# Optimization experiments

Measured on AMD Instinct MI355X. Metric: run time of the kernel, lower is better.

The kernel has to match this reference:

```python
import jax, jax.numpy as jnp
import numpy as np

B, S, D = 4, 1024, 1024
H, DK, DV = 16, 64, 64


def setup_inputs() -> dict:
    key = jax.random.key(0)
    ks = jax.random.split(key, 8)
    sc = 0.02
    return {
        "queries": jax.random.normal(ks[0], (B, S, D), jnp.float32),
        "keys": jax.random.normal(ks[1], (B, S, D), jnp.float32),
        "values": jax.random.normal(ks[2], (B, S, D), jnp.float32),
        "attn_bias": jax.random.normal(ks[3], (B, 1, S, S), jnp.float32),
        "Wq": jax.random.normal(ks[4], (H * DK, D), jnp.float32) * sc,
        "Wk": jax.random.normal(ks[5], (H * DK, D), jnp.float32) * sc,
        "Wv": jax.random.normal(ks[6], (H * DV, D), jnp.float32) * sc,
        "Wp": jax.random.normal(ks[7], (D, H * DV), jnp.float32) * sc,
    }


def reference(queries, keys, values, attn_bias, Wq, Wk, Wv, Wp):
    # Linear (no bias): x @ W.T, then split heads -> [B, H, S, d]
    q = (queries @ Wq.T).reshape(B, S, H, DK).transpose(0, 2, 1, 3)
    k = (keys @ Wk.T).reshape(B, S, H, DK).transpose(0, 2, 1, 3)
    v = (values @ Wv.T).reshape(B, S, H, DV).transpose(0, 2, 1, 3)
    # NOTE: original scales by d_model**-0.5, not d_key**-0.5
    scores = jnp.einsum("bhqd,bhkd->bhqk", q, k) * (D ** -0.5)
    scores = scores + attn_bias  # bias broadcasts over heads
    weights = jax.nn.softmax(scores, axis=-1)
    out = jnp.einsum("bhqk,bhkd->bhqd", weights, v)  # [B,H,S,DV]
    out = out.transpose(0, 2, 1, 3).reshape(B, S, H * DV)
    return out @ Wp.T
```

## Files before the change

kernel.cpp:

```cpp
#include <hip/hip_runtime.h>
#include <hip/hip_bf16.h>

typedef unsigned short u16;
typedef unsigned int u32;
typedef __attribute__((ext_vector_type(8))) short bf16x8;
typedef __attribute__((ext_vector_type(8))) u16 u16x8;
typedef __attribute__((ext_vector_type(4))) u16 u16x4;
typedef __attribute__((ext_vector_type(4))) u32 u32x4;
typedef __attribute__((ext_vector_type(4))) float f32x4;
typedef __attribute__((ext_vector_type(16))) float f32x16;

typedef const __attribute__((address_space(1))) void* gas1_t;
typedef __attribute__((address_space(3))) void* las3_t;

#define MFMA16(a,b,c) __builtin_amdgcn_mfma_f32_16x16x32_bf16((a),(b),(c),0,0,0)
#define MFMA32(a,b,c) __builtin_amdgcn_mfma_f32_32x32x16_bf16((a),(b),(c),0,0,0)

static constexpr int BB = 4, SS = 1024, DD = 1024, HH = 16;

static __device__ __forceinline__ u16 f2b(float x) {
  union { __hip_bfloat16 h; u16 u; } cv;
  cv.h = __float2bfloat16(x);
  return cv.u;
}
static __device__ __forceinline__ u32 pk2(float a, float b) {
  return (u32)f2b(a) | ((u32)f2b(b) << 16);
}

__global__ __launch_bounds__(256) void cvt_all(
    const float* __restrict__ q, const float* __restrict__ k, const float* __restrict__ v,
    const float* __restrict__ wq_, const float* __restrict__ wk_, const float* __restrict__ wv_,
    const float* __restrict__ wp_,
    u16* __restrict__ qb, u16* __restrict__ kb, u16* __restrict__ vb,
    u16* __restrict__ wqb, u16* __restrict__ wkb, u16* __restrict__ wvb, u16* __restrict__ wpb) {
  int bid = blockIdx.x;
  const float* s; u16* d; int off;
  if      (bid < 4096)  { s = q;   d = qb;  off = bid; }
  else if (bid < 8192)  { s = k;   d = kb;  off = bid - 4096; }
  else if (bid < 12288) { s = v;   d = vb;  off = bid - 8192; }
  else if (bid < 13312) { s = wq_; d = wqb; off = bid - 12288; }
  else if (bid < 14336) { s = wk_; d = wkb; off = bid - 13312; }
  else if (bid < 15360) { s = wv_; d = wvb; off = bid - 14336; }
  else                  { s = wp_; d = wpb; off = bid - 15360; }
  int i = (off * 256 + threadIdx.x) * 4;
  float4 val = *(const float4*)(s + i);
  u16x4 r = { f2b(val.x), f2b(val.y), f2b(val.z), f2b(val.w) };
  *(u16x4*)(d + i) = r;
}

template<typename OT>
__global__ __launch_bounds__(256) void gemm_bt(
    const u16* __restrict__ Abase, const u16* __restrict__ Wbase, OT* __restrict__ Cbase,
    int N, int K, size_t sA, size_t sW, size_t sC) {
  const u16* A = Abase + (size_t)blockIdx.z * sA;
  const u16* W = Wbase + (size_t)blockIdx.z * sW;
  OT* C = Cbase + (size_t)blockIdx.z * sC;

  __shared__ __align__(16) u16 As[128 * 32];
  __shared__ __align__(16) u16 Bs[128 * 32];

  const int tid = threadIdx.x;
  const int lane = tid & 63;
  const int wid = tid >> 6;
  const int g = lane >> 4;
  const int li = lane & 15;
  const int brow = blockIdx.y * 128;
  const int bcol = blockIdx.x * 128;
  const int wr = (wid >> 1) * 64;
  const int wc = (wid & 1) * 64;

  const int srow = tid >> 2;
  const int scol = (tid & 3) * 8;

  f32x4 acc[4][4] = {};

  for (int k0 = 0; k0 < K; k0 += 32) {
#pragma unroll
    for (int c = 0; c < 2; ++c) {
      const u16* ga = A + (size_t)(brow + srow + c * 64) * K + k0 + scol;
      const u16* gw = W + (size_t)(bcol + srow + c * 64) * K + k0 + scol;
      __builtin_amdgcn_global_load_lds((gas1_t)(const void*)ga,
                                       (las3_t)(void*)(As + wid * 512 + c * 2048), 16, 0, 0);
      __builtin_amdgcn_global_load_lds((gas1_t)(const void*)gw,
                                       (las3_t)(void*)(Bs + wid * 512 + c * 2048), 16, 0, 0);
    }
    __syncthreads();

    bf16x8 a[4], b[4];
#pragma unroll
    for (int m = 0; m < 4; ++m)
      a[m] = *(const bf16x8*)&As[(wr + m * 16 + li) * 32 + g * 8];
#pragma unroll
    for (int n = 0; n < 4; ++n)
      b[n] = *(const bf16x8*)&Bs[(wc + n * 16 + li) * 32 + g * 8];
#pragma unroll
    for (int m = 0; m < 4; ++m)
#pragma unroll
      for (int n = 0; n < 4; ++n)
        acc[m][n] = MFMA16(a[m], b[n], acc[m][n]);
    __syncthreads();
  }

#pragma unroll
  for (int m = 0; m < 4; ++m)
#pragma unroll
    for (int n = 0; n < 4; ++n)
#pragma unroll
      for (int j = 0; j < 4; ++j) {
        int r = brow + wr + m * 16 + g * 4 + j;
        int c = bcol + wc + n * 16 + li;
        if constexpr (sizeof(OT) == 2) C[(size_t)r * N + c] = (OT)f2b(acc[m][n][j]);
        else                           C[(size_t)r * N + c] = acc[m][n][j];
      }
}

__global__ __launch_bounds__(256) void transpose_v(const u16* __restrict__ V, u16* __restrict__ Vt) {
  __shared__ __align__(16) u16 t[64][72];
  const int s0 = blockIdx.x * 64, h = blockIdx.y, b = blockIdx.z;
  const int tid = threadIdx.x;
#pragma unroll
  for (int it = 0; it < 2; ++it) {
    int slot = tid + it * 256;
    int r = slot >> 3, seg = slot & 7;
    *(u16x8*)&t[r][seg * 8] = *(const u16x8*)&V[(size_t)(b * SS + s0 + r) * DD + h * 64 + seg * 8];
  }
  __syncthreads();
#pragma unroll
  for (int it = 0; it < 2; ++it) {
    int slot = tid + it * 256;
    int dv = slot >> 3, seg = slot & 7;
    u16x8 v;
#pragma unroll
    for (int i = 0; i < 8; ++i) v[i] = t[seg * 8 + i][dv];
    *(u16x8*)&Vt[(size_t)((b * HH + h) * 64 + dv) * SS + s0 + seg * 8] = v;
  }
}

__global__ __launch_bounds__(256) void attn_kernel(
    const u16* __restrict__ Q, const u16* __restrict__ K, const u16* __restrict__ Vt,
    const float* __restrict__ bias, u16* __restrict__ O) {
  __shared__ __align__(16) u16 kbuf[2][64 * 64];
  __shared__ __align__(16) u16 vbuf[2][64 * 64];
  __shared__ float Lf[4][32];

  const int tid = threadIdx.x;
  const int lane = tid & 63;
  const int wq = tid >> 6;
  const int hi = lane >> 5;
  const int ln = lane & 31;
  const u32 swz = (u32)(ln & 7) << 4;
  const int h = blockIdx.y, b = blockIdx.z;
  const int q0 = blockIdx.x * 128;
  const int qrow = q0 + wq * 32 + ln;

  bf16x8 qf[4];
  {
    const u16* qp = Q + (size_t)(b * SS + qrow) * DD + h * 64 + hi * 8;
#pragma unroll
    for (int d = 0; d < 4; ++d) qf[d] = *(const bf16x8*)(qp + d * 16);
  }

  const int sr = tid >> 2;
  const int scb = (tid & 3) * 32;
  const u16* kg = K + (size_t)(b * SS + sr) * DD + h * 64 + scb / 2;
  const u16* vg = Vt + (size_t)((b * HH + h) * 64 + sr) * SS + scb / 2;
  const u32 wa0 = (u32)sr * 128 + (((u32)scb) ^ ((u32)(sr & 7) << 4));
  const u32 wa1 = (u32)sr * 128 + (((u32)scb + 16) ^ ((u32)(sr & 7) << 4));

  u16x8 kr0, kr1, vr0, vr1;
  kr0 = *(const u16x8*)(kg + 0);
  kr1 = *(const u16x8*)(kg + 8);
  vr0 = *(const u16x8*)(vg + 0);
  vr1 = *(const u16x8*)(vg + 8);
  *(u16x8*)((char*)kbuf[0] + wa0) = kr0;
  *(u16x8*)((char*)kbuf[0] + wa1) = kr1;
  *(u16x8*)((char*)vbuf[0] + wa0) = vr0;
  *(u16x8*)((char*)vbuf[0] + wa1) = vr1;
  __syncthreads();

  f32x16 o0 = {}, o1 = {};
  float m = -1e30f, lsum = 0.f;
  int cur = 0;

  for (int kt = 0; kt < 16; ++kt) {
    if (kt < 15) {
      const size_t k1 = (size_t)(kt + 1) * 64;
      kr0 = *(const u16x8*)(kg + k1 * DD + 0);
      kr1 = *(const u16x8*)(kg + k1 * DD + 8);
      vr0 = *(const u16x8*)(vg + k1 + 0);
      vr1 = *(const u16x8*)(vg + k1 + 8);
    }

    f32x4 bb[2][4];
    {
      const float* bp = bias + (size_t)(b * SS + qrow) * SS + kt * 64 + hi * 4;
#pragma unroll
      for (int kb = 0; kb < 2; ++kb)
#pragma unroll
        for (int rq = 0; rq < 4; ++rq)
          bb[kb][rq] = *(const f32x4*)(bp + kb * 32 + rq * 8);
    }

    const char* kb_base = (const char*)kbuf[cur];
    f32x16 s[2];
#pragma unroll
    for (int kb = 0; kb < 2; ++kb) {
      f32x16 acc = {};
#pragma unroll
      for (int d = 0; d < 4; ++d) {
        bf16x8 kf = *(const bf16x8*)(kb_base + (kb * 32 + ln) * 128 + (((u32)(d * 32 + hi * 16)) ^ swz));
        acc = MFMA32(kf, qf[d], acc);
      }
      s[kb] = acc;
    }
#pragma unroll
    for (int kb = 0; kb < 2; ++kb)
#pragma unroll
      for (int rq = 0; rq < 4; ++rq)
#pragma unroll
        for (int c = 0; c < 4; ++c)
          s[kb][rq * 4 + c] = fmaf(s[kb][rq * 4 + c], 0.03125f, bb[kb][rq][c]);

    float mt = -1e30f;
#pragma unroll
    for (int r = 0; r < 16; ++r) { mt = fmaxf(mt, s[0][r]); mt = fmaxf(mt, s[1][r]); }
    mt = fmaxf(mt, __shfl_xor(mt, 32));

    bool resc = false;
    float fsc = 1.f;
    if (kt == 0) {
      m = mt;
    } else if (__any(mt > m + 8.f)) {
      float mn = fmaxf(m, mt);
      fsc = __expf(m - mn);
      m = mn;
      resc = true;
    }

    float rs = 0.f;
    u32 w[2][8];
#pragma unroll
    for (int kb = 0; kb < 2; ++kb)
#pragma unroll
      for (int t = 0; t < 8; ++t) {
        float p0 = __expf(s[kb][2 * t] - m);
        float p1 = __expf(s[kb][2 * t + 1] - m);
        rs += p0 + p1;
        w[kb][t] = pk2(p0, p1);
      }
    rs += __shfl_xor(rs, 32);
    lsum = lsum * fsc + rs;

    if (resc) {
      if (hi == 0) Lf[wq][ln] = fsc;
#pragma unroll
      for (int rq = 0; rq < 4; ++rq) {
        f32x4 fv = *(const f32x4*)&Lf[wq][rq * 8 + hi * 4];
#pragma unroll
        for (int c = 0; c < 4; ++c) { o0[rq * 4 + c] *= fv[c]; o1[rq * 4 + c] *= fv[c]; }
      }
    }

    const char* vb_base = (const char*)vbuf[cur];
#pragma unroll
    for (int ks = 0; ks < 4; ++ks) {
      const int kb = ks >> 1, i0 = (ks & 1) * 4;
      u32 sA = hi ? w[kb][i0 + 0] : w[kb][i0 + 2];
      u32 sB = hi ? w[kb][i0 + 1] : w[kb][i0 + 3];
      u32 rA = (u32)__shfl_xor((int)sA, 32);
      u32 rB = (u32)__shfl_xor((int)sB, 32);
      u32 e0 = hi ? rA : w[kb][i0 + 0];
      u32 e1 = hi ? rB : w[kb][i0 + 1];
      u32 e2 = hi ? w[kb][i0 + 2] : rA;
      u32 e3 = hi ? w[kb][i0 + 3] : rB;
      union { u32x4 u; bf16x8 v; } pc;
      pc.u = (u32x4){e0, e1, e2, e3};
      bf16x8 pa = pc.v;
#pragma unroll
      for (int nv = 0; nv < 2; ++nv) {
        bf16x8 vf = *(const bf16x8*)(vb_base + (nv * 32 + ln) * 128 + (((u32)(ks * 32 + hi * 16)) ^ swz));
        if (nv == 0) o0 = MFMA32(pa, vf, o0);
        else         o1 = MFMA32(pa, vf, o1);
      }
    }

    if (kt < 15) {
      char* kd = (char*)kbuf[cur ^ 1];
      char* vd = (char*)vbuf[cur ^ 1];
      *(u16x8*)(kd + wa0) = kr0;
      *(u16x8*)(kd + wa1) = kr1;
      *(u16x8*)(vd + wa0) = vr0;
      *(u16x8*)(vd + wa1) = vr1;
      __syncthreads();
      cur ^= 1;
    }
  }

  float inv = 1.0f / lsum;
  if (hi == 0) Lf[wq][ln] = inv;
#pragma unroll
  for (int rq = 0; rq < 4; ++rq) {
    f32x4 iv = *(const f32x4*)&Lf[wq][rq * 8 + hi * 4];
#pragma unroll
    for (int c = 0; c < 4; ++c) {
      int q = q0 + wq * 32 + rq * 8 + hi * 4 + c;
      u16* op = O + (size_t)(b * SS + q) * DD + h * 64 + ln;
      op[0]  = f2b(o0[rq * 4 + c] * iv[c]);
      op[32] = f2b(o1[rq * 4 + c] * iv[c]);
    }
  }
}

extern "C" void kernel_launch(void* const* d_in, const int* in_sizes, int n_in,
                              void* d_out, int out_size, void* d_ws, size_t ws_size,
                              hipStream_t stream) {
  const float* queries = (const float*)d_in[0];
  const float* keys    = (const float*)d_in[1];
  const float* values  = (const float*)d_in[2];
  const float* bias    = (const float*)d_in[3];
  const float* Wq      = (const float*)d_in[4];
  const float* Wk      = (const float*)d_in[5];
  const float* Wv      = (const float*)d_in[6];
  const float* Wp      = (const float*)d_in[7];
  float* out = (float*)d_out;

  char* ws = (char*)d_ws;
  const size_t MB = 1024 * 1024;
  u16* qb  = (u16*)(ws + 0 * MB);
  u16* kb  = (u16*)(ws + 8 * MB);
  u16* vb  = (u16*)(ws + 16 * MB);
  u16* wqb = (u16*)(ws + 24 * MB);
  u16* wkb = (u16*)(ws + 26 * MB);
  u16* wvb = (u16*)(ws + 28 * MB);
  u16* wpb = (u16*)(ws + 30 * MB);
  u16* Qb  = (u16*)(ws + 32 * MB);
  u16* Kb  = (u16*)(ws + 40 * MB);
  u16* Vb  = (u16*)(ws + 48 * MB);
  u16* Vtb = (u16*)(ws + 56 * MB);
  u16* Ob  = (u16*)(ws + 0 * MB);

  const int nAct = BB * SS * DD;
  const int nW = DD * DD;

  cvt_all<<<dim3(16384), dim3(256), 0, stream>>>(
      queries, keys, values, Wq, Wk, Wv, Wp,
      qb, kb, vb, wqb, wkb, wvb, wpb);

  gemm_bt<u16><<<dim3(8, 32, 3), dim3(256), 0, stream>>>(
      qb, wqb, Qb, DD, DD, (size_t)nAct, (size_t)nW, (size_t)nAct);

  transpose_v<<<dim3(16, 16, 4), dim3(256), 0, stream>>>(Vb, Vtb);

  attn_kernel<<<dim3(8, 16, 4), dim3(256), 0, stream>>>(Qb, Kb, Vtb, bias, Ob);

  gemm_bt<float><<<dim3(8, 32, 1), dim3(256), 0, stream>>>(
      Ob, wpb, out, DD, DD, 0, 0, 0);
}
```

Measured before the change: 139.8 us.

## Stage attention bias tiles through LDS with direct global-to-LDS loads and remap blocks

The attention kernel now loads each 128x64 fp32 bias tile with global_load_lds into a swizzled LDS buffer, using coalesced row reads instead of strided per-lane vector loads. Each thread then reads its bias values from LDS after a barrier. Block indices are remapped so that consecutive blocks spread across heads and batches. Per-row softmax rescale and normalization factors now move through cross-lane shuffles instead of an LDS scratch array. In exchange the kernel uses 32KB more LDS, which may lower occupancy, and adds a barrier in every iteration.

```diff
diff --git a/kernel.cpp b/kernel.cpp
--- a/kernel.cpp
+++ b/kernel.cpp
@@ -141,7 +141,7 @@
     const float* __restrict__ bias, u16* __restrict__ O) {
   __shared__ __align__(16) u16 kbuf[2][64 * 64];
   __shared__ __align__(16) u16 vbuf[2][64 * 64];
-  __shared__ float Lf[4][32];
+  __shared__ __align__(16) float bbuf[8192];
 
   const int tid = threadIdx.x;
   const int lane = tid & 63;
@@ -149,8 +149,11 @@
   const int hi = lane >> 5;
   const int ln = lane & 31;
   const u32 swz = (u32)(ln & 7) << 4;
-  const int h = blockIdx.y, b = blockIdx.z;
-  const int q0 = blockIdx.x * 128;
+
+  const int flat = blockIdx.x + (blockIdx.y << 3) + (blockIdx.z << 7);
+  const int L = ((flat & 7) << 6) | (flat >> 3);
+  const int qt = L & 7, h = (L >> 3) & 15, b = L >> 7;
+  const int q0 = qt * 128;
   const int qrow = q0 + wq * 32 + ln;
 
   bf16x8 qf[4];
@@ -166,6 +169,20 @@
   const u16* vg = Vt + (size_t)((b * HH + h) * 64 + sr) * SS + scb / 2;
   const u32 wa0 = (u32)sr * 128 + (((u32)scb) ^ ((u32)(sr & 7) << 4));
   const u32 wa1 = (u32)sr * 128 + (((u32)scb + 16) ^ ((u32)(sr & 7) << 4));
+
+  const int brow_ = tid >> 4;
+  const int bgl = (tid & 15) ^ (brow_ & 15);
+  const float* bsrc = bias + (size_t)(b * SS + q0 + brow_) * SS + bgl * 4;
+  char* bdst = (char*)bbuf + wq * 1024;
+
+  const int qq = wq * 32 + ln;
+  const char* bb_base = (const char*)bbuf + qq * 256;
+  int baddr[2][4];
+#pragma unroll
+  for (int kb = 0; kb < 2; ++kb)
+#pragma unroll
+    for (int rq = 0; rq < 4; ++rq)
+      baddr[kb][rq] = ((kb * 8 + rq * 2 + hi) ^ (qq & 15)) << 4;
 
   u16x8 kr0, kr1, vr0, vr1;
   kr0 = *(const u16x8*)(kg + 0);
@@ -183,6 +200,13 @@
   int cur = 0;
 
   for (int kt = 0; kt < 16; ++kt) {
+    {
+      const float* bs = bsrc + kt * 64;
+#pragma unroll
+      for (int i = 0; i < 8; ++i)
+        __builtin_amdgcn_global_load_lds((gas1_t)(const void*)(bs + i * 16384),
+                                         (las3_t)(void*)(bdst + i * 4096), 16, 0, 0);
+    }
     if (kt < 15) {
       const size_t k1 = (size_t)(kt + 1) * 64;
       kr0 = *(const u16x8*)(kg + k1 * DD + 0);
@@ -191,16 +215,6 @@
       vr1 = *(const u16x8*)(vg + k1 + 8);
     }
 
-    f32x4 bb[2][4];
-    {
-      const float* bp = bias + (size_t)(b * SS + qrow) * SS + kt * 64 + hi * 4;
-#pragma unroll
-      for (int kb = 0; kb < 2; ++kb)
-#pragma unroll
-        for (int rq = 0; rq < 4; ++rq)
-          bb[kb][rq] = *(const f32x4*)(bp + kb * 32 + rq * 8);
-    }
-
     const char* kb_base = (const char*)kbuf[cur];
     f32x16 s[2];
 #pragma unroll
@@ -213,13 +227,18 @@
       }
       s[kb] = acc;
     }
+
+    __syncthreads();
+
 #pragma unroll
     for (int kb = 0; kb < 2; ++kb)
 #pragma unroll
-      for (int rq = 0; rq < 4; ++rq)
+      for (int rq = 0; rq < 4; ++rq) {
+        f32x4 bbv = *(const f32x4*)(bb_base + baddr[kb][rq]);
 #pragma unroll
         for (int c = 0; c < 4; ++c)
-          s[kb][rq * 4 + c] = fmaf(s[kb][rq * 4 + c], 0.03125f, bb[kb][rq][c]);
+          s[kb][rq * 4 + c] = fmaf(s[kb][rq * 4 + c], 0.03125f, bbv[c]);
+      }
 
     float mt = -1e30f;
 #pragma unroll
@@ -238,7 +257,7 @@
     }
 
     float rs = 0.f;
-    u32 w[2][8];
+    u32 wv[2][8];
 #pragma unroll
     for (int kb = 0; kb < 2; ++kb)
 #pragma unroll
@@ -246,18 +265,16 @@
         float p0 = __expf(s[kb][2 * t] - m);
         float p1 = __expf(s[kb][2 * t + 1] - m);
         rs += p0 + p1;
-        w[kb][t] = pk2(p0, p1);
+        wv[kb][t] = pk2(p0, p1);
       }
     rs += __shfl_xor(rs, 32);
     lsum = lsum * fsc + rs;
 
     if (resc) {
-      if (hi == 0) Lf[wq][ln] = fsc;
-#pragma unroll
-      for (int rq = 0; rq < 4; ++rq) {
-        f32x4 fv = *(const f32x4*)&Lf[wq][rq * 8 + hi * 4];
-#pragma unroll
-        for (int c = 0; c < 4; ++c) { o0[rq * 4 + c] *= fv[c]; o1[rq * 4 + c] *= fv[c]; }
+#pragma unroll
+      for (int j = 0; j < 16; ++j) {
+        float fv = __shfl(fsc, (j & 3) + 8 * (j >> 2) + 4 * hi);
+        o0[j] *= fv; o1[j] *= fv;
       }
     }
 
@@ -265,14 +282,14 @@
 #pragma unroll
     for (int ks = 0; ks < 4; ++ks) {
       const int kb = ks >> 1, i0 = (ks & 1) * 4;
-      u32 sA = hi ? w[kb][i0 + 0] : w[kb][i0 + 2];
-      u32 sB = hi ? w[kb][i0 + 1] : w[kb][i0 + 3];
+      u32 sA = hi ? wv[kb][i0 + 0] : wv[kb][i0 + 2];
+      u32 sB = hi ? wv[kb][i0 + 1] : wv[kb][i0 + 3];
       u32 rA = (u32)__shfl_xor((int)sA, 32);
       u32 rB = (u32)__shfl_xor((int)sB, 32);
-      u32 e0 = hi ? rA : w[kb][i0 + 0];
-      u32 e1 = hi ? rB : w[kb][i0 + 1];
-      u32 e2 = hi ? w[kb][i0 + 2] : rA;
-      u32 e3 = hi ? w[kb][i0 + 3] : rB;
+      u32 e0 = hi ? rA : wv[kb][i0 + 0];
+      u32 e1 = hi ? rB : wv[kb][i0 + 1];
+      u32 e2 = hi ? wv[kb][i0 + 2] : rA;
+      u32 e3 = hi ? wv[kb][i0 + 3] : rB;
       union { u32x4 u; bf16x8 v; } pc;
       pc.u = (u32x4){e0, e1, e2, e3};
       bf16x8 pa = pc.v;
@@ -291,23 +308,19 @@
       *(u16x8*)(kd + wa1) = kr1;
       *(u16x8*)(vd + wa0) = vr0;
       *(u16x8*)(vd + wa1) = vr1;
-      __syncthreads();
-      cur ^= 1;
-    }
+    }
+    __syncthreads();
+    cur ^= 1;
   }
 
   float inv = 1.0f / lsum;
-  if (hi == 0) Lf[wq][ln] = inv;
-#pragma unroll
-  for (int rq = 0; rq < 4; ++rq) {
-    f32x4 iv = *(const f32x4*)&Lf[wq][rq * 8 + hi * 4];
-#pragma unroll
-    for (int c = 0; c < 4; ++c) {
-      int q = q0 + wq * 32 + rq * 8 + hi * 4 + c;
-      u16* op = O + (size_t)(b * SS + q) * DD + h * 64 + ln;
-      op[0]  = f2b(o0[rq * 4 + c] * iv[c]);
-      op[32] = f2b(o1[rq * 4 + c] * iv[c]);
-    }
+#pragma unroll
+  for (int j = 0; j < 16; ++j) {
+    float iv = __shfl(inv, (j & 3) + 8 * (j >> 2) + 4 * hi);
+    int q = q0 + wq * 32 + (j & 3) + 8 * (j >> 2) + 4 * hi;
+    u16* op = O + (size_t)(b * SS + q) * DD + h * 64 + ln;
+    op[0]  = f2b(o0[j] * iv);
+    op[32] = f2b(o1[j] * iv);
   }
 }
 
```

Measured after the change: 134.5 us. 3.8% less time.
